# Kernel tuning notes

Measured on AMD Instinct MI355X. Metric: run time of the kernel, lower is better.

Reference implementation:

```python
import jax, jax.numpy as jnp
import numpy as np

D_IN = 2048
D_OUT = 2048
NUM_HEADS = 16
NUM_KV_GROUPS = 4
GROUP_SIZE = NUM_HEADS // NUM_KV_GROUPS  # 4
HEAD_DIM = D_OUT // NUM_HEADS            # 128


def setup_inputs() -> dict:
    key = jax.random.key(0)
    ks = jax.random.split(key, 6)
    b, n = 2, 2048
    x = jax.random.normal(ks[0], (b, n, D_IN), dtype=jnp.float32)
    # weights stored as [in, out] so that x @ W matches torch's x @ weight.T
    Wq = jax.random.normal(ks[1], (D_IN, D_OUT), dtype=jnp.float32) * (1.0 / np.sqrt(D_IN))
    Wk = jax.random.normal(ks[2], (D_IN, NUM_KV_GROUPS * HEAD_DIM), dtype=jnp.float32) * (1.0 / np.sqrt(D_IN))
    Wv = jax.random.normal(ks[3], (D_IN, NUM_KV_GROUPS * HEAD_DIM), dtype=jnp.float32) * (1.0 / np.sqrt(D_IN))
    Wo = jax.random.normal(ks[4], (D_OUT, D_OUT), dtype=jnp.float32) * (1.0 / np.sqrt(D_OUT))
    bo = jax.random.normal(ks[5], (D_OUT,), dtype=jnp.float32) * 0.01
    return {"x": x, "Wq": Wq, "Wk": Wk, "Wv": Wv, "Wo": Wo, "bo": bo}


def reference(x, Wq, Wk, Wv, Wo, bo):
    b, n, _ = x.shape
    # projections
    q = (x @ Wq).reshape(b, n, NUM_KV_GROUPS, GROUP_SIZE, HEAD_DIM)  # [b,n,g,s,d]
    k = (x @ Wk).reshape(b, n, NUM_KV_GROUPS, HEAD_DIM)              # [b,n,g,d]
    v = (x @ Wv).reshape(b, n, NUM_KV_GROUPS, HEAD_DIM)
    scale = 1.0 / np.sqrt(HEAD_DIM).astype(np.float32)
    # scores: each group of GROUP_SIZE query heads shares one K/V head
    scores = jnp.einsum('bqgsd,bkgd->bgsqk', q, k) * scale  # [b,g,s,n,n]
    causal = jnp.arange(n)[:, None] < jnp.arange(n)[None, :]  # True above diagonal
    scores = jnp.where(causal, -jnp.inf, scores)
    attn = jax.nn.softmax(scores, axis=-1)
    # dropout omitted for determinism (eval-mode equivalent)
    ctx = jnp.einsum('bgsqk,bkgd->bqgsd', attn, v)  # [b,n,g,s,d]
    ctx = ctx.reshape(b, n, D_OUT)
    return ctx @ Wo + bo
```

## Files before the change

kernel.cpp:

```cpp
#include <hip/hip_runtime.h>
#include <hip/hip_bf16.h>

typedef short bf16x8 __attribute__((ext_vector_type(8)));
typedef float f32x4 __attribute__((ext_vector_type(4)));
typedef float f32x16 __attribute__((ext_vector_type(16)));
typedef unsigned int u32x4 __attribute__((ext_vector_type(4)));

#define MFMA16(a, b, c) __builtin_amdgcn_mfma_f32_16x16x32_bf16((a), (b), (c), 0, 0, 0)
#define MFMA32(a, b, c) __builtin_amdgcn_mfma_f32_32x32x16_bf16((a), (b), (c), 0, 0, 0)

static __device__ __forceinline__ unsigned short f2bf(float f) {
  union { float f; unsigned u; } v;
  v.f = f;
  unsigned r = (v.u + 0x7FFFu + ((v.u >> 16) & 1u)) >> 16;
  return (unsigned short)r;
}

static __device__ __forceinline__ void gload16(const void* g, void* l) {
  __builtin_amdgcn_global_load_lds(
      (const __attribute__((address_space(1))) unsigned int*)g,
      (__attribute__((address_space(3))) unsigned int*)l, 16, 0, 0);
}

__global__ __launch_bounds__(256) void cast_f32_bf16(
    const float* __restrict__ src, unsigned short* __restrict__ dst, int n4) {
  int stride = gridDim.x * blockDim.x;
  for (int i = blockIdx.x * blockDim.x + threadIdx.x; i < n4; i += stride) {
    float4 v = reinterpret_cast<const float4*>(src)[i];
    ushort4 o;
    o.x = f2bf(v.x); o.y = f2bf(v.y); o.z = f2bf(v.z); o.w = f2bf(v.w);
    reinterpret_cast<ushort4*>(dst)[i] = o;
  }
}

__global__ __launch_bounds__(256) void transpose_cast(
    const float* __restrict__ src, unsigned short* __restrict__ dst, int R, int C) {
  __shared__ float tile[32][33];
  int tx = threadIdx.x & 31;
  int ty = threadIdx.x >> 5;
  int r0 = blockIdx.y * 32, c0 = blockIdx.x * 32;
#pragma unroll
  for (int i = 0; i < 32; i += 8)
    tile[ty + i][tx] = src[(size_t)(r0 + ty + i) * C + (c0 + tx)];
  __syncthreads();
#pragma unroll
  for (int i = 0; i < 32; i += 8)
    dst[(size_t)(c0 + ty + i) * R + (r0 + tx)] = f2bf(tile[tx][ty + i]);
}

template <int EPI>
static __device__ __forceinline__ void gemm_core(
    unsigned short* Asm, unsigned short* Bsm,
    const unsigned short* __restrict__ A, const unsigned short* __restrict__ B,
    unsigned short* __restrict__ Cb, float* __restrict__ Cf,
    const float* __restrict__ bias, int N, int K, int bid) {
  const int tid = threadIdx.x;
  const int wave = tid >> 6;
  const int lane = tid & 63;
  const int l15 = lane & 15, l4 = lane >> 4;
  const int tilesN = N >> 7;
  const int bm = bid / tilesN, bn = bid % tilesN;
  const int row0 = bm << 7, col0 = bn << 7;
  const int wr = (wave >> 1) << 6, wc = (wave & 1) << 6;

  const int ch0 = wave * 128 + lane;
  const int ch1 = ch0 + 64;
  const int r_a0 = ch0 >> 2, k_a0 = (ch0 & 3) * 8;
  const int r_a1 = ch1 >> 2, k_a1 = (ch1 & 3) * 8;

  f32x4 acc[4][4] = {};

  for (int kt = 0; kt < K; kt += 32) {
    if (kt) __syncthreads();
    gload16(A + (size_t)(row0 + r_a0) * K + kt + k_a0, &Asm[(wave * 2 + 0) * 512]);
    gload16(A + (size_t)(row0 + r_a1) * K + kt + k_a1, &Asm[(wave * 2 + 1) * 512]);
    gload16(B + (size_t)(col0 + r_a0) * K + kt + k_a0, &Bsm[(wave * 2 + 0) * 512]);
    gload16(B + (size_t)(col0 + r_a1) * K + kt + k_a1, &Bsm[(wave * 2 + 1) * 512]);
    __syncthreads();

    bf16x8 af[4], bvf[4];
#pragma unroll
    for (int m = 0; m < 4; ++m)
      af[m] = *(const bf16x8*)&Asm[(wr + m * 16 + l15) * 32 + l4 * 8];
#pragma unroll
    for (int n = 0; n < 4; ++n)
      bvf[n] = *(const bf16x8*)&Bsm[(wc + n * 16 + l15) * 32 + l4 * 8];
#pragma unroll
    for (int m = 0; m < 4; ++m)
#pragma unroll
      for (int n = 0; n < 4; ++n)
        acc[m][n] = MFMA16(af[m], bvf[n], acc[m][n]);
  }

#pragma unroll
  for (int m = 0; m < 4; ++m) {
#pragma unroll
    for (int n = 0; n < 4; ++n) {
      int row = row0 + wr + m * 16 + l4 * 4;
      int col = col0 + wc + n * 16 + l15;
#pragma unroll
      for (int r = 0; r < 4; ++r) {
        if (EPI == 0) {
          Cb[(size_t)(row + r) * N + col] = f2bf(acc[m][n][r]);
        } else {
          Cf[(size_t)(row + r) * N + col] = acc[m][n][r] + bias[col];
        }
      }
    }
  }
}

__global__ __launch_bounds__(256) void gemm_dual(
    const unsigned short* __restrict__ A1, const unsigned short* __restrict__ B1,
    unsigned short* __restrict__ C1,
    const unsigned short* __restrict__ A2, const unsigned short* __restrict__ B2,
    unsigned short* __restrict__ C2, int K) {
  __shared__ unsigned short Asm[128 * 32];
  __shared__ unsigned short Bsm[128 * 32];
  if (blockIdx.x < 128)
    gemm_core<0>(Asm, Bsm, A1, B1, C1, nullptr, nullptr, 512, K, blockIdx.x);
  else
    gemm_core<0>(Asm, Bsm, A2, B2, C2, nullptr, nullptr, 4096, K, blockIdx.x - 128);
}

template <int EPI>
__global__ __launch_bounds__(512, 2) void gemm8p(
    const unsigned short* __restrict__ A, const unsigned short* __restrict__ B,
    unsigned short* __restrict__ Cb, float* __restrict__ Cf,
    const float* __restrict__ bias, int N, int K) {
  __shared__ unsigned short Al[3][256 * 64];
  __shared__ unsigned short Bl[3][128 * 64];
  const int tid = threadIdx.x;
  const int wave = tid >> 6, lane = tid & 63;
  const int l15 = lane & 15, l4 = lane >> 4;
  const int tilesN = N >> 7;
  const int bm = blockIdx.x / tilesN, bn = blockIdx.x % tilesN;
  const int row0 = bm << 8, col0 = bn << 7;
  const int wr = (wave >> 1) << 6;
  const int wc = (wave & 1) << 6;

  const unsigned short* sA[4];
  const unsigned short* sB[2];
#pragma unroll
  for (int i = 0; i < 4; ++i) {
    int q = i * 512 + wave * 64 + lane;
    int r = q >> 3, c = (q & 7) ^ (r & 7);
    sA[i] = A + (size_t)(row0 + r) * K + c * 8;
  }
#pragma unroll
  for (int i = 0; i < 2; ++i) {
    int q = i * 512 + wave * 64 + lane;
    int r = q >> 3, c = (q & 7) ^ (r & 7);
    sB[i] = B + (size_t)(col0 + r) * K + c * 8;
  }

#define STG_H1(t_, bi)                                             \
  { const size_t ko = (size_t)(t_) * 64;                           \
    gload16(sA[0] + ko, &Al[bi][(0 * 512 + wave * 64) * 8]);       \
    gload16(sA[1] + ko, &Al[bi][(1 * 512 + wave * 64) * 8]);       \
    gload16(sB[0] + ko, &Bl[bi][(0 * 512 + wave * 64) * 8]); }
#define STG_H2(t_, bi)                                             \
  { const size_t ko = (size_t)(t_) * 64;                           \
    gload16(sA[2] + ko, &Al[bi][(2 * 512 + wave * 64) * 8]);       \
    gload16(sA[3] + ko, &Al[bi][(3 * 512 + wave * 64) * 8]);       \
    gload16(sB[1] + ko, &Bl[bi][(1 * 512 + wave * 64) * 8]); }

  const int sw = l15 & 7;
  const int c0 = (l4 ^ sw) << 4;
  const int c1 = ((4 + l4) ^ sw) << 4;
  const int rbA = (wr + l15) << 7;
  const int rbB = (wc + l15) << 7;

  f32x4 acc[4][4] = {};
  const int NT = K >> 6;

  STG_H1(0, 0); STG_H2(0, 0);
  STG_H1(1, 1); STG_H2(1, 1);

  int cur = 0;
  for (int t = 0; t < NT; ++t) {
    int sb = cur + 2; if (sb >= 3) sb -= 3;
    if (t + 1 < NT) { asm volatile("s_waitcnt vmcnt(6)" ::: "memory"); }
    else            { asm volatile("s_waitcnt vmcnt(0)" ::: "memory"); }
    __builtin_amdgcn_s_barrier();
    asm volatile("" ::: "memory");
    const char* Ab = (const char*)&Al[cur][0];
    const char* Bb = (const char*)&Bl[cur][0];
    bf16x8 b0[4], b1[4], aA[2][2], aB[2][2];
#pragma unroll
    for (int n = 0; n < 4; ++n) {
      b0[n] = *(const bf16x8*)(Bb + rbB + n * 2048 + c0);
      b1[n] = *(const bf16x8*)(Bb + rbB + n * 2048 + c1);
    }
#pragma unroll
    for (int m = 0; m < 2; ++m) {
      aA[m][0] = *(const bf16x8*)(Ab + rbA + m * 2048 + c0);
      aA[m][1] = *(const bf16x8*)(Ab + rbA + m * 2048 + c1);
    }
    if (t + 2 < NT) STG_H1(t + 2, sb);
    asm volatile("" ::: "memory");
    __builtin_amdgcn_s_barrier();
    asm volatile("" ::: "memory");
    __builtin_amdgcn_s_setprio(1);
#pragma unroll
    for (int m = 0; m < 2; ++m)
#pragma unroll
      for (int n = 0; n < 4; ++n) {
        acc[m][n] = MFMA16(aA[m][0], b0[n], acc[m][n]);
        acc[m][n] = MFMA16(aA[m][1], b1[n], acc[m][n]);
      }
    __builtin_amdgcn_s_setprio(0);
#pragma unroll
    for (int m = 0; m < 2; ++m) {
      aB[m][0] = *(const bf16x8*)(Ab + rbA + (m + 2) * 2048 + c0);
      aB[m][1] = *(const bf16x8*)(Ab + rbA + (m + 2) * 2048 + c1);
    }
    if (t + 2 < NT) STG_H2(t + 2, sb);
    asm volatile("" ::: "memory");
    __builtin_amdgcn_s_barrier();
    asm volatile("" ::: "memory");
    __builtin_amdgcn_s_setprio(1);
#pragma unroll
    for (int m = 0; m < 2; ++m)
#pragma unroll
      for (int n = 0; n < 4; ++n) {
        acc[m + 2][n] = MFMA16(aB[m][0], b0[n], acc[m + 2][n]);
        acc[m + 2][n] = MFMA16(aB[m][1], b1[n], acc[m + 2][n]);
      }
    __builtin_amdgcn_s_setprio(0);
    cur += 1; if (cur >= 3) cur = 0;
  }
#undef STG_H1
#undef STG_H2

#pragma unroll
  for (int m = 0; m < 4; ++m) {
#pragma unroll
    for (int n = 0; n < 4; ++n) {
      int row = row0 + wr + m * 16 + l4 * 4;
      int col = col0 + wc + n * 16 + l15;
#pragma unroll
      for (int r = 0; r < 4; ++r) {
        if (EPI == 0) {
          Cb[(size_t)(row + r) * N + col] = f2bf(acc[m][n][r]);
        } else {
          Cf[(size_t)(row + r) * N + col] = acc[m][n][r] + bias[col];
        }
      }
    }
  }
}

__global__ __launch_bounds__(256, 3) void flash_gqa5(
    const unsigned short* __restrict__ Qb, const unsigned short* __restrict__ Kb,
    const unsigned short* __restrict__ VT, unsigned short* __restrict__ Ctx) {
  __shared__ unsigned short Sm[16384];

  const int tid = threadIdx.x;
  const int wave = tid >> 6, lane = tid & 63;
  const int l31 = lane & 31, hi = lane >> 5;
  const int i = blockIdx.x >> 3;
  const int bg = blockIdx.x & 7;
  const int qt = (i < 32) ? i : (95 - i);
  const int b = bg >> 2, g = bg & 3;
  const int h = (g << 2) | wave;
  const int q0 = qt << 5;
  const int T = qt + 1;

  bf16x8 qf[8];
  {
    const unsigned short* qp =
        Qb + (size_t)(b * 2048 + q0 + l31) * 2048 + h * 128 + hi * 8;
#pragma unroll
    for (int ds = 0; ds < 8; ++ds) qf[ds] = *(const bf16x8*)(qp + ds * 16);
  }

  const int rK0 = tid >> 4, cK = tid & 15, rK1 = rK0 + 16;
  const unsigned short* kSA =
      Kb + (size_t)(b * 2048 + rK0) * 512 + g * 128 + (cK ^ (rK0 & 7)) * 8;
  const unsigned short* kSB =
      Kb + (size_t)(b * 2048 + rK1) * 512 + g * 128 + (cK ^ (rK1 & 7)) * 8;
  const int rV0 = tid >> 2, cV = tid & 3, rV1 = rV0 + 64;
  const unsigned short* vSA =
      VT + (size_t)(g * 128 + rV0) * 4096 + b * 2048 + (cV ^ (rV0 & 3)) * 8;
  const unsigned short* vSB =
      VT + (size_t)(g * 128 + rV1) * 4096 + b * 2048 + (cV ^ (rV1 & 3)) * 8;

  const float scale = 0.08838834764831845f;

#define STAGE5(t_, bi)                                          \
  {                                                             \
    unsigned short* kb_ = Sm + (bi)*8192;                       \
    unsigned short* vb_ = kb_ + 4096;                           \
    const size_t ko_ = (size_t)(t_) * 32;                       \
    gload16(kSA + ko_ * 512, kb_ + wave * 512);                 \
    gload16(kSB + ko_ * 512, kb_ + 2048 + wave * 512);          \
    gload16(vSA + ko_, vb_ + wave * 512);                       \
    gload16(vSB + ko_, vb_ + 2048 + wave * 512);                \
  }

  float m_r = -1e30f, l_r = 0.f;
  f32x16 o0 = {}, o1 = {}, o2 = {}, o3 = {};

  STAGE5(0, 0);
  __syncthreads();

  for (int t = 0; t < T; ++t) {
    const int buf = t & 1;
    if (t + 1 < T) STAGE5(t + 1, buf ^ 1);
    const char* Kl = (const char*)Sm + buf * 16384;
    const char* Vl = Kl + 8192;
    const int kv = t << 5;
    f32x16 st = {};
    __builtin_amdgcn_s_setprio(1);
#pragma unroll
    for (int ds = 0; ds < 8; ++ds) {
      const int by = (l31 * 256 + ds * 32 + hi * 16) ^ ((l31 & 7) << 4);
      bf16x8 kf = *(const bf16x8*)(Kl + by);
      st = MFMA32(kf, qf[ds], st);
    }
    __builtin_amdgcn_s_setprio(0);
    if (t == qt) {
      const int q_abs = q0 + l31;
#pragma unroll
      for (int rr = 0; rr < 16; ++rr) {
        const int koff = (rr & 3) + 8 * (rr >> 2) + 4 * hi;
        st[rr] = (kv + koff <= q_abs) ? st[rr] * scale : -1e30f;
      }
    } else {
#pragma unroll
      for (int rr = 0; rr < 16; ++rr) st[rr] *= scale;
    }
    float pm = st[0];
#pragma unroll
    for (int rr = 1; rr < 16; ++rr) pm = fmaxf(pm, st[rr]);
    pm = fmaxf(pm, __shfl_xor(pm, 32));
    if (!__all(pm - m_r <= 8.0f)) {
      const float mn = fmaxf(m_r, pm);
      const float osc = __expf(m_r - mn);
      m_r = mn;
      l_r *= osc;
#pragma unroll
      for (int rr = 0; rr < 16; ++rr) {
        o0[rr] *= osc; o1[rr] *= osc; o2[rr] *= osc; o3[rr] *= osc;
      }
    }
    float ps = 0.f;
#pragma unroll
    for (int rr = 0; rr < 16; ++rr) { st[rr] = __expf(st[rr] - m_r); ps += st[rr]; }
    ps += __shfl_xor(ps, 32);
    l_r += ps;
    unsigned w[8];
#pragma unroll
    for (int rp = 0; rp < 8; ++rp)
      w[rp] = (unsigned)f2bf(st[2 * rp]) | ((unsigned)f2bf(st[2 * rp + 1]) << 16);
    __builtin_amdgcn_s_setprio(1);
#define PV_KS(ks)                                                             \
    {                                                                         \
      const int k4 = (ks)*4;                                                  \
      unsigned a0 = w[k4], a1 = w[k4 + 1], b0 = w[k4 + 2], b1 = w[k4 + 3];    \
      unsigned q0_ = hi ? a0 : b0, q1_ = hi ? a1 : b1;                        \
      unsigned e0 = (unsigned)__shfl_xor((int)q0_, 32);                       \
      unsigned e1 = (unsigned)__shfl_xor((int)q1_, 32);                       \
      union { u32x4 u; bf16x8 v; } pk;                                        \
      pk.u[0] = hi ? e0 : a0; pk.u[1] = hi ? e1 : a1;                         \
      pk.u[2] = hi ? b0 : e0; pk.u[3] = hi ? b1 : e1;                         \
      const int cb = (ks)*32 + hi * 16;                                       \
      { const int row = l31;      const int by = (row * 64 + cb) ^ ((row & 3) << 4); \
        bf16x8 vf = *(const bf16x8*)(Vl + by); o0 = MFMA32(vf, pk.v, o0); }   \
      { const int row = 32 + l31; const int by = (row * 64 + cb) ^ ((row & 3) << 4); \
        bf16x8 vf = *(const bf16x8*)(Vl + by); o1 = MFMA32(vf, pk.v, o1); }   \
      { const int row = 64 + l31; const int by = (row * 64 + cb) ^ ((row & 3) << 4); \
        bf16x8 vf = *(const bf16x8*)(Vl + by); o2 = MFMA32(vf, pk.v, o2); }   \
      { const int row = 96 + l31; const int by = (row * 64 + cb) ^ ((row & 3) << 4); \
        bf16x8 vf = *(const bf16x8*)(Vl + by); o3 = MFMA32(vf, pk.v, o3); }   \
    }
    PV_KS(0) PV_KS(1)
#undef PV_KS
    __builtin_amdgcn_s_setprio(0);
    __syncthreads();
  }
#undef STAGE5

  const float inv = 1.f / l_r;
  unsigned short* cp = Ctx + (size_t)(b * 2048 + q0 + l31) * 2048 + h * 128;
#pragma unroll
  for (int a = 0; a < 4; ++a) {
    ushort4 p0, p1, p2, p3;
    p0.x = f2bf(o0[4 * a + 0] * inv); p0.y = f2bf(o0[4 * a + 1] * inv);
    p0.z = f2bf(o0[4 * a + 2] * inv); p0.w = f2bf(o0[4 * a + 3] * inv);
    p1.x = f2bf(o1[4 * a + 0] * inv); p1.y = f2bf(o1[4 * a + 1] * inv);
    p1.z = f2bf(o1[4 * a + 2] * inv); p1.w = f2bf(o1[4 * a + 3] * inv);
    p2.x = f2bf(o2[4 * a + 0] * inv); p2.y = f2bf(o2[4 * a + 1] * inv);
    p2.z = f2bf(o2[4 * a + 2] * inv); p2.w = f2bf(o2[4 * a + 3] * inv);
    p3.x = f2bf(o3[4 * a + 0] * inv); p3.y = f2bf(o3[4 * a + 1] * inv);
    p3.z = f2bf(o3[4 * a + 2] * inv); p3.w = f2bf(o3[4 * a + 3] * inv);
    const int cc = 8 * a + 4 * hi;
    *(ushort4*)(cp + 0 * 32 + cc) = p0;
    *(ushort4*)(cp + 1 * 32 + cc) = p1;
    *(ushort4*)(cp + 2 * 32 + cc) = p2;
    *(ushort4*)(cp + 3 * 32 + cc) = p3;
  }
}

extern "C" void kernel_launch(void* const* d_in, const int* in_sizes, int n_in,
                              void* d_out, int out_size, void* d_ws, size_t ws_size,
                              hipStream_t stream) {
  (void)in_sizes; (void)n_in; (void)out_size; (void)ws_size;
  const float* x  = (const float*)d_in[0];
  const float* Wq = (const float*)d_in[1];
  const float* Wk = (const float*)d_in[2];
  const float* Wv = (const float*)d_in[3];
  const float* Wo = (const float*)d_in[4];
  const float* bo = (const float*)d_in[5];
  float* out = (float*)d_out;

  unsigned short* Xb  = (unsigned short*)d_ws;
  unsigned short* WqT = Xb  + (size_t)4096 * 2048;
  unsigned short* WkT = WqT + (size_t)2048 * 2048;
  unsigned short* WvT = WkT + (size_t)512 * 2048;
  unsigned short* WoT = WvT + (size_t)512 * 2048;
  unsigned short* Qb  = WoT + (size_t)2048 * 2048;
  unsigned short* Kb  = Qb  + (size_t)4096 * 2048;
  unsigned short* VTb = Kb  + (size_t)4096 * 512;
  unsigned short* Ctx = VTb + (size_t)512 * 4096;

  cast_f32_bf16<<<2048, 256, 0, stream>>>(x, Xb, (4096 * 2048) / 4);
  transpose_cast<<<dim3(64, 64), 256, 0, stream>>>(Wq, WqT, 2048, 2048);
  transpose_cast<<<dim3(16, 64), 256, 0, stream>>>(Wk, WkT, 2048, 512);
  transpose_cast<<<dim3(16, 64), 256, 0, stream>>>(Wv, WvT, 2048, 512);
  transpose_cast<<<dim3(64, 64), 256, 0, stream>>>(Wo, WoT, 2048, 2048);

  gemm8p<0><<<dim3(256), 512, 0, stream>>>(Xb, WqT, Qb, nullptr, nullptr, 2048, 2048);
  gemm_dual<<<dim3(256), 256, 0, stream>>>(Xb, WkT, Kb, WvT, Xb, VTb, 2048);

  flash_gqa5<<<dim3(512), 256, 0, stream>>>(Qb, Kb, VTb, Ctx);

  gemm8p<1><<<dim3(256), 512, 0, stream>>>(Ctx, WoT, nullptr, out, bo, 2048, 2048);
}
```

Before: 220.4 us.

## Fuse weight prep and QKV projections, restage V tiles, use exp2 softmax

Merges the four weight transpose-cast launches into one kernel. Fuses the Q, K and V^T projections into a single 8-wave pipelined GEMM launch, relying on WkT sitting directly after WqT in memory so Q and K form one wide GEMM. The old small-tile dual GEMM is dropped. The flash kernel now stages V in 64-key chunks with an 8-way swizzle, folds log2(e) into the scale to use exp2f, widens the lazy-rescale threshold, and uses a cheaper round-to-nearest bf16 pack. This uses more LDS, and the flash kernel's occupancy hint drops from 3 to 2 blocks.

```diff
diff --git a/kernel.cpp b/kernel.cpp
--- a/kernel.cpp
+++ b/kernel.cpp
@@ -14,6 +14,12 @@
   v.f = f;
   unsigned r = (v.u + 0x7FFFu + ((v.u >> 16) & 1u)) >> 16;
   return (unsigned short)r;
+}
+
+static __device__ __forceinline__ unsigned pk2(float a, float b) {
+  unsigned ua = __float_as_uint(a) + 0x8000u;
+  unsigned ub = __float_as_uint(b) + 0x8000u;
+  return (ua >> 16) | (ub & 0xFFFF0000u);
 }
 
 static __device__ __forceinline__ void gload16(const void* g, void* l) {
@@ -33,12 +39,21 @@
   }
 }
 
-__global__ __launch_bounds__(256) void transpose_cast(
-    const float* __restrict__ src, unsigned short* __restrict__ dst, int R, int C) {
+__global__ __launch_bounds__(256) void prep_all(
+    const float* __restrict__ Wq, const float* __restrict__ Wk,
+    const float* __restrict__ Wv, const float* __restrict__ Wo,
+    unsigned short* __restrict__ WqT, unsigned short* __restrict__ WkT,
+    unsigned short* __restrict__ WvT, unsigned short* __restrict__ WoT) {
   __shared__ float tile[32][33];
+  int id = blockIdx.x;
+  const float* src; unsigned short* dst; int R, C, bx, by;
+  if (id < 4096)      { src = Wq; dst = WqT; R = 2048; C = 2048; bx = id & 63; by = id >> 6; }
+  else if (id < 5120) { id -= 4096; src = Wk; dst = WkT; R = 2048; C = 512; bx = id & 15; by = id >> 4; }
+  else if (id < 6144) { id -= 5120; src = Wv; dst = WvT; R = 2048; C = 512; bx = id & 15; by = id >> 4; }
+  else                { id -= 6144; src = Wo; dst = WoT; R = 2048; C = 2048; bx = id & 63; by = id >> 6; }
   int tx = threadIdx.x & 31;
   int ty = threadIdx.x >> 5;
-  int r0 = blockIdx.y * 32, c0 = blockIdx.x * 32;
+  int r0 = by * 32, c0 = bx * 32;
 #pragma unroll
   for (int i = 0; i < 32; i += 8)
     tile[ty + i][tx] = src[(size_t)(r0 + ty + i) * C + (c0 + tx)];
@@ -49,92 +64,16 @@
 }
 
 template <int EPI>
-static __device__ __forceinline__ void gemm_core(
-    unsigned short* Asm, unsigned short* Bsm,
+static __device__ __forceinline__ void g8p_core(
     const unsigned short* __restrict__ A, const unsigned short* __restrict__ B,
-    unsigned short* __restrict__ Cb, float* __restrict__ Cf,
-    const float* __restrict__ bias, int N, int K, int bid) {
-  const int tid = threadIdx.x;
-  const int wave = tid >> 6;
-  const int lane = tid & 63;
-  const int l15 = lane & 15, l4 = lane >> 4;
-  const int tilesN = N >> 7;
-  const int bm = bid / tilesN, bn = bid % tilesN;
-  const int row0 = bm << 7, col0 = bn << 7;
-  const int wr = (wave >> 1) << 6, wc = (wave & 1) << 6;
-
-  const int ch0 = wave * 128 + lane;
-  const int ch1 = ch0 + 64;
-  const int r_a0 = ch0 >> 2, k_a0 = (ch0 & 3) * 8;
-  const int r_a1 = ch1 >> 2, k_a1 = (ch1 & 3) * 8;
-
-  f32x4 acc[4][4] = {};
-
-  for (int kt = 0; kt < K; kt += 32) {
-    if (kt) __syncthreads();
-    gload16(A + (size_t)(row0 + r_a0) * K + kt + k_a0, &Asm[(wave * 2 + 0) * 512]);
-    gload16(A + (size_t)(row0 + r_a1) * K + kt + k_a1, &Asm[(wave * 2 + 1) * 512]);
-    gload16(B + (size_t)(col0 + r_a0) * K + kt + k_a0, &Bsm[(wave * 2 + 0) * 512]);
-    gload16(B + (size_t)(col0 + r_a1) * K + kt + k_a1, &Bsm[(wave * 2 + 1) * 512]);
-    __syncthreads();
-
-    bf16x8 af[4], bvf[4];
-#pragma unroll
-    for (int m = 0; m < 4; ++m)
-      af[m] = *(const bf16x8*)&Asm[(wr + m * 16 + l15) * 32 + l4 * 8];
-#pragma unroll
-    for (int n = 0; n < 4; ++n)
-      bvf[n] = *(const bf16x8*)&Bsm[(wc + n * 16 + l15) * 32 + l4 * 8];
-#pragma unroll
-    for (int m = 0; m < 4; ++m)
-#pragma unroll
-      for (int n = 0; n < 4; ++n)
-        acc[m][n] = MFMA16(af[m], bvf[n], acc[m][n]);
-  }
-
-#pragma unroll
-  for (int m = 0; m < 4; ++m) {
-#pragma unroll
-    for (int n = 0; n < 4; ++n) {
-      int row = row0 + wr + m * 16 + l4 * 4;
-      int col = col0 + wc + n * 16 + l15;
-#pragma unroll
-      for (int r = 0; r < 4; ++r) {
-        if (EPI == 0) {
-          Cb[(size_t)(row + r) * N + col] = f2bf(acc[m][n][r]);
-        } else {
-          Cf[(size_t)(row + r) * N + col] = acc[m][n][r] + bias[col];
-        }
-      }
-    }
-  }
-}
-
-__global__ __launch_bounds__(256) void gemm_dual(
-    const unsigned short* __restrict__ A1, const unsigned short* __restrict__ B1,
-    unsigned short* __restrict__ C1,
-    const unsigned short* __restrict__ A2, const unsigned short* __restrict__ B2,
-    unsigned short* __restrict__ C2, int K) {
-  __shared__ unsigned short Asm[128 * 32];
-  __shared__ unsigned short Bsm[128 * 32];
-  if (blockIdx.x < 128)
-    gemm_core<0>(Asm, Bsm, A1, B1, C1, nullptr, nullptr, 512, K, blockIdx.x);
-  else
-    gemm_core<0>(Asm, Bsm, A2, B2, C2, nullptr, nullptr, 4096, K, blockIdx.x - 128);
-}
-
-template <int EPI>
-__global__ __launch_bounds__(512, 2) void gemm8p(
-    const unsigned short* __restrict__ A, const unsigned short* __restrict__ B,
-    unsigned short* __restrict__ Cb, float* __restrict__ Cf,
-    const float* __restrict__ bias, int N, int K) {
-  __shared__ unsigned short Al[3][256 * 64];
-  __shared__ unsigned short Bl[3][128 * 64];
+    unsigned short* __restrict__ Cb, unsigned short* __restrict__ Cb2,
+    float* __restrict__ Cf, const float* __restrict__ bias,
+    int N, int K, int bid, unsigned short* Al, unsigned short* Bl) {
   const int tid = threadIdx.x;
   const int wave = tid >> 6, lane = tid & 63;
   const int l15 = lane & 15, l4 = lane >> 4;
   const int tilesN = N >> 7;
-  const int bm = blockIdx.x / tilesN, bn = blockIdx.x % tilesN;
+  const int bm = bid / tilesN, bn = bid % tilesN;
   const int row0 = bm << 8, col0 = bn << 7;
   const int wr = (wave >> 1) << 6;
   const int wc = (wave & 1) << 6;
@@ -154,16 +93,16 @@
     sB[i] = B + (size_t)(col0 + r) * K + c * 8;
   }
 
-#define STG_H1(t_, bi)                                             \
-  { const size_t ko = (size_t)(t_) * 64;                           \
-    gload16(sA[0] + ko, &Al[bi][(0 * 512 + wave * 64) * 8]);       \
-    gload16(sA[1] + ko, &Al[bi][(1 * 512 + wave * 64) * 8]);       \
-    gload16(sB[0] + ko, &Bl[bi][(0 * 512 + wave * 64) * 8]); }
-#define STG_H2(t_, bi)                                             \
-  { const size_t ko = (size_t)(t_) * 64;                           \
-    gload16(sA[2] + ko, &Al[bi][(2 * 512 + wave * 64) * 8]);       \
-    gload16(sA[3] + ko, &Al[bi][(3 * 512 + wave * 64) * 8]);       \
-    gload16(sB[1] + ko, &Bl[bi][(1 * 512 + wave * 64) * 8]); }
+#define STG_H1(t_, bi)                                                      \
+  { const size_t ko = (size_t)(t_) * 64;                                    \
+    gload16(sA[0] + ko, &Al[(bi)*16384 + (0 * 512 + wave * 64) * 8]);       \
+    gload16(sA[1] + ko, &Al[(bi)*16384 + (1 * 512 + wave * 64) * 8]);       \
+    gload16(sB[0] + ko, &Bl[(bi)*8192 + (0 * 512 + wave * 64) * 8]); }
+#define STG_H2(t_, bi)                                                      \
+  { const size_t ko = (size_t)(t_) * 64;                                    \
+    gload16(sA[2] + ko, &Al[(bi)*16384 + (2 * 512 + wave * 64) * 8]);       \
+    gload16(sA[3] + ko, &Al[(bi)*16384 + (3 * 512 + wave * 64) * 8]);       \
+    gload16(sB[1] + ko, &Bl[(bi)*8192 + (1 * 512 + wave * 64) * 8]); }
 
   const int sw = l15 & 7;
   const int c0 = (l4 ^ sw) << 4;
@@ -184,8 +123,8 @@
     else            { asm volatile("s_waitcnt vmcnt(0)" ::: "memory"); }
     __builtin_amdgcn_s_barrier();
     asm volatile("" ::: "memory");
-    const char* Ab = (const char*)&Al[cur][0];
-    const char* Bb = (const char*)&Bl[cur][0];
+    const char* Ab = (const char*)&Al[cur * 16384];
+    const char* Bb = (const char*)&Bl[cur * 8192];
     bf16x8 b0[4], b1[4], aA[2][2], aB[2][2];
 #pragma unroll
     for (int n = 0; n < 4; ++n) {
@@ -243,18 +182,41 @@
       for (int r = 0; r < 4; ++r) {
         if (EPI == 0) {
           Cb[(size_t)(row + r) * N + col] = f2bf(acc[m][n][r]);
+        } else if (EPI == 1) {
+          Cf[(size_t)(row + r) * N + col] = acc[m][n][r] + bias[col];
         } else {
-          Cf[(size_t)(row + r) * N + col] = acc[m][n][r] + bias[col];
+          if (col < 2048) Cb[(size_t)(row + r) * 2048 + col] = f2bf(acc[m][n][r]);
+          else            Cb2[(size_t)(row + r) * 512 + col - 2048] = f2bf(acc[m][n][r]);
         }
       }
     }
   }
 }
 
-__global__ __launch_bounds__(256, 3) void flash_gqa5(
+__global__ __launch_bounds__(512, 2) void gemm8p_o(
+    const unsigned short* __restrict__ A, const unsigned short* __restrict__ B,
+    float* __restrict__ Cf, const float* __restrict__ bias, int N, int K) {
+  __shared__ unsigned short Al[3 * 256 * 64];
+  __shared__ unsigned short Bl[3 * 128 * 64];
+  g8p_core<1>(A, B, nullptr, nullptr, Cf, bias, N, K, blockIdx.x, Al, Bl);
+}
+
+__global__ __launch_bounds__(512, 2) void gemm_fused3(
+    const unsigned short* __restrict__ Xb, const unsigned short* __restrict__ Bqk,
+    unsigned short* __restrict__ Qb, unsigned short* __restrict__ Kb,
+    const unsigned short* __restrict__ WvT, unsigned short* __restrict__ VTb) {
+  __shared__ unsigned short Al[3 * 256 * 64];
+  __shared__ unsigned short Bl[3 * 128 * 64];
+  if (blockIdx.x < 320)
+    g8p_core<2>(Xb, Bqk, Qb, Kb, nullptr, nullptr, 2560, 2048, blockIdx.x, Al, Bl);
+  else
+    g8p_core<0>(WvT, Xb, VTb, nullptr, nullptr, nullptr, 4096, 2048, blockIdx.x - 320, Al, Bl);
+}
+
+__global__ __launch_bounds__(256, 2) void flash_gqa6(
     const unsigned short* __restrict__ Qb, const unsigned short* __restrict__ Kb,
     const unsigned short* __restrict__ VT, unsigned short* __restrict__ Ctx) {
-  __shared__ unsigned short Sm[16384];
+  __shared__ unsigned short Sm[24576];
 
   const int tid = threadIdx.x;
   const int wave = tid >> 6, lane = tid & 63;
@@ -280,36 +242,49 @@
       Kb + (size_t)(b * 2048 + rK0) * 512 + g * 128 + (cK ^ (rK0 & 7)) * 8;
   const unsigned short* kSB =
       Kb + (size_t)(b * 2048 + rK1) * 512 + g * 128 + (cK ^ (rK1 & 7)) * 8;
-  const int rV0 = tid >> 2, cV = tid & 3, rV1 = rV0 + 64;
-  const unsigned short* vSA =
-      VT + (size_t)(g * 128 + rV0) * 4096 + b * 2048 + (cV ^ (rV0 & 3)) * 8;
-  const unsigned short* vSB =
-      VT + (size_t)(g * 128 + rV1) * 4096 + b * 2048 + (cV ^ (rV1 & 3)) * 8;
-
-  const float scale = 0.08838834764831845f;
-
-#define STAGE5(t_, bi)                                          \
-  {                                                             \
-    unsigned short* kb_ = Sm + (bi)*8192;                       \
-    unsigned short* vb_ = kb_ + 4096;                           \
-    const size_t ko_ = (size_t)(t_) * 32;                       \
-    gload16(kSA + ko_ * 512, kb_ + wave * 512);                 \
-    gload16(kSB + ko_ * 512, kb_ + 2048 + wave * 512);          \
-    gload16(vSA + ko_, vb_ + wave * 512);                       \
-    gload16(vSB + ko_, vb_ + 2048 + wave * 512);                \
-  }
+  const int cV = tid & 7;
+  const unsigned short* vS[4];
+#pragma unroll
+  for (int c = 0; c < 4; ++c) {
+    int row = c * 32 + (tid >> 3);
+    vS[c] = VT + (size_t)(g * 128 + row) * 4096 + b * 2048 + (cV ^ (row & 7)) * 8;
+  }
+
+#define STAGE_K(t_, bi)                                           \
+  {                                                               \
+    unsigned short* kb_ = Sm + (bi)*4096;                         \
+    const size_t ko_ = (size_t)(t_) * 32 * 512;                   \
+    gload16(kSA + ko_, kb_ + wave * 512);                         \
+    gload16(kSB + ko_, kb_ + 2048 + wave * 512);                  \
+  }
+#define STAGE_V(p_, bi, half)                                     \
+  {                                                               \
+    unsigned short* vb_ = Sm + 8192 + (bi)*8192;                  \
+    const size_t po_ = (size_t)(p_) * 64;                         \
+    const int c_ = (half)*2;                                      \
+    gload16(vS[c_] + po_, vb_ + c_ * 2048 + wave * 512);          \
+    gload16(vS[c_ + 1] + po_, vb_ + (c_ + 1) * 2048 + wave * 512);\
+  }
+
+  const float s2 = 0.12751744f;
 
   float m_r = -1e30f, l_r = 0.f;
   f32x16 o0 = {}, o1 = {}, o2 = {}, o3 = {};
 
-  STAGE5(0, 0);
+  STAGE_K(0, 0);
+  STAGE_V(0, 0, 0);
+  STAGE_V(0, 0, 1);
   __syncthreads();
 
   for (int t = 0; t < T; ++t) {
     const int buf = t & 1;
-    if (t + 1 < T) STAGE5(t + 1, buf ^ 1);
-    const char* Kl = (const char*)Sm + buf * 16384;
-    const char* Vl = Kl + 8192;
+    const int pb = (t >> 1) & 1;
+    if (t + 1 < T) STAGE_K(t + 1, buf ^ 1);
+    const int p1 = (t >> 1) + 1;
+    if (2 * p1 < T) STAGE_V(p1, p1 & 1, t & 1);
+
+    const char* Kl = (const char*)Sm + buf * 8192;
+    const char* Vl = (const char*)Sm + 16384 + pb * 16384;
     const int kv = t << 5;
     f32x16 st = {};
     __builtin_amdgcn_s_setprio(1);
@@ -325,19 +300,19 @@
 #pragma unroll
       for (int rr = 0; rr < 16; ++rr) {
         const int koff = (rr & 3) + 8 * (rr >> 2) + 4 * hi;
-        st[rr] = (kv + koff <= q_abs) ? st[rr] * scale : -1e30f;
+        st[rr] = (kv + koff <= q_abs) ? st[rr] * s2 : -1e30f;
       }
     } else {
 #pragma unroll
-      for (int rr = 0; rr < 16; ++rr) st[rr] *= scale;
+      for (int rr = 0; rr < 16; ++rr) st[rr] *= s2;
     }
     float pm = st[0];
 #pragma unroll
     for (int rr = 1; rr < 16; ++rr) pm = fmaxf(pm, st[rr]);
     pm = fmaxf(pm, __shfl_xor(pm, 32));
-    if (!__all(pm - m_r <= 8.0f)) {
+    if (!__all(pm - m_r <= 11.5f)) {
       const float mn = fmaxf(m_r, pm);
-      const float osc = __expf(m_r - mn);
+      const float osc = exp2f(m_r - mn);
       m_r = mn;
       l_r *= osc;
 #pragma unroll
@@ -347,13 +322,12 @@
     }
     float ps = 0.f;
 #pragma unroll
-    for (int rr = 0; rr < 16; ++rr) { st[rr] = __expf(st[rr] - m_r); ps += st[rr]; }
+    for (int rr = 0; rr < 16; ++rr) { st[rr] = exp2f(st[rr] - m_r); ps += st[rr]; }
     ps += __shfl_xor(ps, 32);
     l_r += ps;
     unsigned w[8];
 #pragma unroll
-    for (int rp = 0; rp < 8; ++rp)
-      w[rp] = (unsigned)f2bf(st[2 * rp]) | ((unsigned)f2bf(st[2 * rp + 1]) << 16);
+    for (int rp = 0; rp < 8; ++rp) w[rp] = pk2(st[2 * rp], st[2 * rp + 1]);
     __builtin_amdgcn_s_setprio(1);
 #define PV_KS(ks)                                                             \
     {                                                                         \
@@ -365,14 +339,14 @@
       union { u32x4 u; bf16x8 v; } pk;                                        \
       pk.u[0] = hi ? e0 : a0; pk.u[1] = hi ? e1 : a1;                         \
       pk.u[2] = hi ? b0 : e0; pk.u[3] = hi ? b1 : e1;                         \
-      const int cb = (ks)*32 + hi * 16;                                       \
-      { const int row = l31;      const int by = (row * 64 + cb) ^ ((row & 3) << 4); \
+      const int cb = (t & 1) * 64 + (ks)*32 + hi * 16;                        \
+      { const int row = l31;      const int by = (row * 128 + cb) ^ ((row & 7) << 4); \
         bf16x8 vf = *(const bf16x8*)(Vl + by); o0 = MFMA32(vf, pk.v, o0); }   \
-      { const int row = 32 + l31; const int by = (row * 64 + cb) ^ ((row & 3) << 4); \
+      { const int row = 32 + l31; const int by = (row * 128 + cb) ^ ((row & 7) << 4); \
         bf16x8 vf = *(const bf16x8*)(Vl + by); o1 = MFMA32(vf, pk.v, o1); }   \
-      { const int row = 64 + l31; const int by = (row * 64 + cb) ^ ((row & 3) << 4); \
+      { const int row = 64 + l31; const int by = (row * 128 + cb) ^ ((row & 7) << 4); \
         bf16x8 vf = *(const bf16x8*)(Vl + by); o2 = MFMA32(vf, pk.v, o2); }   \
-      { const int row = 96 + l31; const int by = (row * 64 + cb) ^ ((row & 3) << 4); \
+      { const int row = 96 + l31; const int by = (row * 128 + cb) ^ ((row & 7) << 4); \
         bf16x8 vf = *(const bf16x8*)(Vl + by); o3 = MFMA32(vf, pk.v, o3); }   \
     }
     PV_KS(0) PV_KS(1)
@@ -380,7 +354,8 @@
     __builtin_amdgcn_s_setprio(0);
     __syncthreads();
   }
-#undef STAGE5
+#undef STAGE_K
+#undef STAGE_V
 
   const float inv = 1.f / l_r;
   unsigned short* cp = Ctx + (size_t)(b * 2048 + q0 + l31) * 2048 + h * 128;
@@ -426,15 +401,11 @@
   unsigned short* Ctx = VTb + (size_t)512 * 4096;
 
   cast_f32_bf16<<<2048, 256, 0, stream>>>(x, Xb, (4096 * 2048) / 4);
-  transpose_cast<<<dim3(64, 64), 256, 0, stream>>>(Wq, WqT, 2048, 2048);
-  transpose_cast<<<dim3(16, 64), 256, 0, stream>>>(Wk, WkT, 2048, 512);
-  transpose_cast<<<dim3(16, 64), 256, 0, stream>>>(Wv, WvT, 2048, 512);
-  transpose_cast<<<dim3(64, 64), 256, 0, stream>>>(Wo, WoT, 2048, 2048);
-
-  gemm8p<0><<<dim3(256), 512, 0, stream>>>(Xb, WqT, Qb, nullptr, nullptr, 2048, 2048);
-  gemm_dual<<<dim3(256), 256, 0, stream>>>(Xb, WkT, Kb, WvT, Xb, VTb, 2048);
-
-  flash_gqa5<<<dim3(512), 256, 0, stream>>>(Qb, Kb, VTb, Ctx);
-
-  gemm8p<1><<<dim3(256), 512, 0, stream>>>(Ctx, WoT, nullptr, out, bo, 2048, 2048);
-}
+  prep_all<<<10240, 256, 0, stream>>>(Wq, Wk, Wv, Wo, WqT, WkT, WvT, WoT);
+
+  gemm_fused3<<<dim3(384), 512, 0, stream>>>(Xb, WqT, Qb, Kb, WvT, VTb);
+
+  flash_gqa6<<<dim3(512), 256, 0, stream>>>(Qb, Kb, VTb, Ctx);
+
+  gemm8p_o<<<dim3(256), 512, 0, stream>>>(Ctx, WoT, out, bo, 2048, 2048);
+}
```

New measurement: 209.8 us. -4.8%, faster.
